# Performance work log

Measured on AMD Instinct MI355X. Metric: run time of the kernel, lower is better.

The kernel has to match this reference:

```python
import jax, jax.numpy as jnp
import numpy as np

BATCH, IN_DIM, LATENT, K = 16384, 768, 12288, 32

def setup_inputs() -> dict:
    key = jax.random.key(0)
    k1, k2, k3 = jax.random.split(key, 3)
    # kaiming-uniform-style scale for encoder/decoder weights
    enc_bound = float(np.sqrt(6.0 / IN_DIM))
    dec_bound = float(np.sqrt(6.0 / LATENT))
    x = jax.random.normal(k1, (BATCH, IN_DIM), dtype=jnp.float32)
    enc_w = jax.random.uniform(k2, (LATENT, IN_DIM), dtype=jnp.float32, minval=-enc_bound, maxval=enc_bound)
    enc_b = jnp.zeros((LATENT,), dtype=jnp.float32)
    dec_w = jax.random.uniform(k3, (IN_DIM, LATENT), dtype=jnp.float32, minval=-dec_bound, maxval=dec_bound)
    dec_b = jnp.zeros((IN_DIM,), dtype=jnp.float32)
    return {"x": x, "enc_w": enc_w, "enc_b": enc_b, "dec_w": dec_w, "dec_b": dec_b, "k": K}

def reference(x, enc_w, enc_b, dec_w, dec_b, k):
    # encode: z = x @ W_e^T + b_e            [B, LATENT]
    z = jnp.einsum('bi,li->bl', x, enc_w) + enc_b
    # top-k threshold: kth largest value per row, then shifted relu
    vals, _ = jax.lax.top_k(z, k)
    thresh = vals[:, -1:]                     # [B, 1]
    z_sparse = jax.nn.relu(z - thresh)
    # decode: dense GEMM over all latent columns (as in original module)
    x_recon = jnp.einsum('bl,il->bi', z_sparse, dec_w) + dec_b
    return (x_recon, z_sparse)
```

## Files before the change

### kernel.cpp

```cpp
#include <hip/hip_runtime.h>

#define M_DIM 16384
#define K_DIM 768
#define N_DIM 12288
#define TOPK  32
#define NCHUNK (N_DIM / 128)

typedef float f32x4 __attribute__((ext_vector_type(4)));
typedef short s16x8 __attribute__((ext_vector_type(8)));

__device__ __forceinline__ unsigned f2u(float f) {
  union { float f; unsigned u; } v; v.f = f; return v.u;
}
__device__ __forceinline__ float u2f(unsigned u) {
  union { unsigned u; float f; } v; v.u = u; return v.f;
}
__device__ __forceinline__ unsigned fkey(float f) {
  const unsigned u = f2u(f);
  return u ^ (unsigned)(((int)u >> 31) | 0x80000000);
}
__device__ __forceinline__ float kinv(unsigned k) {
  return u2f((k & 0x80000000u) ? (k ^ 0x80000000u) : ~k);
}
__device__ __forceinline__ unsigned short bf16_rne(float f) {
  unsigned u = f2u(f);
  return (unsigned short)((u + 0x7FFFu + ((u >> 16) & 1u)) >> 16);
}

__global__ __launch_bounds__(256) void TopKSparseAutoencoder_51917564674099_prep(
    const float* __restrict__ x, const float* __restrict__ w,
    const float* __restrict__ dw,
    unsigned short* __restrict__ xhi, unsigned short* __restrict__ xlo,
    unsigned short* __restrict__ whi, unsigned short* __restrict__ wlo,
    float* __restrict__ WT, int do_t, int do_s)
{
  __shared__ float tile[32][33];
  const int b = (int)blockIdx.x;
  const int t = (int)threadIdx.x;

  if (b < 9216) {
    if (!do_t) return;
    const int bx = b % (N_DIM / 32);
    const int by = b / (N_DIM / 32);
    const int tx = t & 31, ty = t >> 5;
#pragma unroll
    for (int j = 0; j < 32; j += 8)
      tile[ty + j][tx] = dw[(size_t)(by * 32 + ty + j) * N_DIM + bx * 32 + tx];
    __syncthreads();
#pragma unroll
    for (int j = 0; j < 32; j += 8)
      WT[(size_t)(bx * 32 + ty + j) * K_DIM + by * 32 + tx] = tile[tx][ty + j];
    return;
  }
  if (!do_s) return;

  const float* src; unsigned short* dh; unsigned short* dl; int i, stride, n4;
  if (b < 9216 + 1024) {
    src = x; dh = xhi; dl = xlo;
    i = (b - 9216) * 256 + t; stride = 1024 * 256; n4 = M_DIM * K_DIM / 4;
  } else {
    src = w; dh = whi; dl = wlo;
    i = (b - 10240) * 256 + t; stride = 512 * 256; n4 = N_DIM * K_DIM / 4;
  }
  for (; i < n4; i += stride) {
    const float4 v = ((const float4*)src)[i];
    ushort4 h, l;
    h.x = bf16_rne(v.x); h.y = bf16_rne(v.y); h.z = bf16_rne(v.z); h.w = bf16_rne(v.w);
    l.x = bf16_rne(v.x - u2f((unsigned)h.x << 16));
    l.y = bf16_rne(v.y - u2f((unsigned)h.y << 16));
    l.z = bf16_rne(v.z - u2f((unsigned)h.z << 16));
    l.w = bf16_rne(v.w - u2f((unsigned)h.w << 16));
    ((ushort4*)dh)[i] = h;
    ((ushort4*)dl)[i] = l;
  }
}

__device__ __forceinline__ void mfma16(f32x4& d, s16x8 a, s16x8 b) {
  asm("v_mfma_f32_16x16x32_bf16 %0, %1, %2, %0" : "+v"(d) : "v"(a), "v"(b));
}

#define GL16(g, l) __builtin_amdgcn_global_load_lds(                      \
    (const __attribute__((address_space(1))) void*)(g),                   \
    (__attribute__((address_space(3))) void*)(l), 16, 0, 0)

__global__ __launch_bounds__(256, 2) void TopKSparseAutoencoder_51917564674099_kernel(
    const unsigned short* __restrict__ Ahi, const unsigned short* __restrict__ Alo,
    const unsigned short* __restrict__ Bhi, const unsigned short* __restrict__ Blo,
    const float* __restrict__ bias, float* __restrict__ Z,
    float* __restrict__ cmax, int do_cmax)
{
  __shared__ unsigned short lds[4][128][32];
  __shared__ float cmx[128][2];

  const int t    = (int)threadIdx.x;
  const int wid  = t >> 6;
  const int lane = t & 63;

  const int bid  = (int)(blockIdx.y * gridDim.x + blockIdx.x);
  const int bswz = (bid & 7) * (12288 / 8) + (bid >> 3);
  const int n0   = (bswz % 96) * 128;
  const int m0   = (bswz / 96) * 128;

  const int rr  = lane >> 2;
  const int kq  = lane & 3;
  const int rt0 = wid * 32 + rr;
  const int rt1 = rt0 + 16;
  const int kc0 = (kq ^ ((rt0 >> 1) & 3)) * 8;
  const int kc1 = (kq ^ ((rt1 >> 1) & 3)) * 8;
  const size_t offA0 = (size_t)(m0 + rt0) * K_DIM + kc0;
  const size_t offA1 = (size_t)(m0 + rt1) * K_DIM + kc1;
  const size_t offB0 = (size_t)(n0 + rt0) * K_DIM + kc0;
  const size_t offB1 = (size_t)(n0 + rt1) * K_DIM + kc1;

  const int wm = (wid >> 1) * 64;
  const int wn = (wid & 1) * 64;
  const int lr = lane & 15;
  const int lc = lane >> 4;

  f32x4 acc[4][4];
#pragma unroll
  for (int i = 0; i < 4; ++i)
#pragma unroll
    for (int j = 0; j < 4; ++j) acc[i][j] = (f32x4){0.f, 0.f, 0.f, 0.f};

  for (int k0 = 0; k0 < K_DIM; k0 += 32) {
    GL16(Ahi + offA0 + k0, &lds[0][wid * 32][0]);
    GL16(Ahi + offA1 + k0, &lds[0][wid * 32 + 16][0]);
    GL16(Alo + offA0 + k0, &lds[1][wid * 32][0]);
    GL16(Alo + offA1 + k0, &lds[1][wid * 32 + 16][0]);
    GL16(Bhi + offB0 + k0, &lds[2][wid * 32][0]);
    GL16(Bhi + offB1 + k0, &lds[2][wid * 32 + 16][0]);
    GL16(Blo + offB0 + k0, &lds[3][wid * 32][0]);
    GL16(Blo + offB1 + k0, &lds[3][wid * 32 + 16][0]);
    __syncthreads();

    s16x8 ah[4], al[4], bh[4], bl[4];
#pragma unroll
    for (int i = 0; i < 4; ++i) {
      const int r = wm + i * 16 + lr;
      const int p = (lc ^ ((r >> 1) & 3)) * 8;
      ah[i] = *(const s16x8*)&lds[0][r][p];
      al[i] = *(const s16x8*)&lds[1][r][p];
    }
#pragma unroll
    for (int j = 0; j < 4; ++j) {
      const int r = wn + j * 16 + lr;
      const int p = (lc ^ ((r >> 1) & 3)) * 8;
      bh[j] = *(const s16x8*)&lds[2][r][p];
      bl[j] = *(const s16x8*)&lds[3][r][p];
    }
#pragma unroll
    for (int i = 0; i < 4; ++i)
#pragma unroll
      for (int j = 0; j < 4; ++j) {
        mfma16(acc[i][j], ah[i], bh[j]);
        mfma16(acc[i][j], ah[i], bl[j]);
        mfma16(acc[i][j], al[i], bh[j]);
      }
    __syncthreads();
  }

  asm volatile("s_nop 7\n\ts_nop 7" :::);

  float mx[4][4];
#pragma unroll
  for (int i = 0; i < 4; ++i)
#pragma unroll
    for (int q = 0; q < 4; ++q) mx[i][q] = -3.4e38f;

#pragma unroll
  for (int j = 0; j < 4; ++j) {
    const int col = n0 + wn + j * 16 + lr;
    const float bb = bias[col];
#pragma unroll
    for (int i = 0; i < 4; ++i) {
      const int r0 = m0 + wm + i * 16 + lc * 4;
#pragma unroll
      for (int q = 0; q < 4; ++q) {
        const float val = acc[i][j][q] + bb;
        Z[(size_t)(r0 + q) * N_DIM + col] = val;
        mx[i][q] = fmaxf(mx[i][q], val);
      }
    }
  }

  if (do_cmax) {
#pragma unroll
    for (int s = 1; s < 16; s <<= 1)
#pragma unroll
      for (int i = 0; i < 4; ++i)
#pragma unroll
        for (int q = 0; q < 4; ++q)
          mx[i][q] = fmaxf(mx[i][q], __shfl_xor(mx[i][q], s));
    if (lr == 0) {
#pragma unroll
      for (int i = 0; i < 4; ++i)
#pragma unroll
        for (int q = 0; q < 4; ++q)
          cmx[wm + i * 16 + lc * 4 + q][wid & 1] = mx[i][q];
    }
    __syncthreads();
    if (t < 128)
      cmax[(size_t)(m0 + t) * NCHUNK + (n0 >> 7)] = fmaxf(cmx[t][0], cmx[t][1]);
  }
}

__global__ void enc_gemm_f32_fb(
    const float* A, const float* B, const float* bias, float* Z)
{
  __shared__ float As[32][132];
  __shared__ float Bs[32][132];

  const int tx = (int)threadIdx.x;
  const int ty = (int)threadIdx.y;
  const int t  = ty * 16 + tx;
  const int n0 = (int)blockIdx.x * 128;
  const int m0 = (int)blockIdx.y * 128;
  const int r = t >> 1;
  const int h = (t & 1) * 16;

  float c[8][8];
#pragma unroll
  for (int i = 0; i < 8; ++i)
#pragma unroll
    for (int j = 0; j < 8; ++j) c[i][j] = 0.0f;

  for (int k0 = 0; k0 < K_DIM; k0 += 32) {
    const float* pa = A + (size_t)(m0 + r) * K_DIM + k0 + h;
    const float* pb = B + (size_t)(n0 + r) * K_DIM + k0 + h;
    float fa[16], fb[16];
#pragma unroll
    for (int j = 0; j < 16; ++j) fa[j] = pa[j];
#pragma unroll
    for (int j = 0; j < 16; ++j) fb[j] = pb[j];
#pragma unroll
    for (int j = 0; j < 16; ++j) As[h + j][r] = fa[j];
#pragma unroll
    for (int j = 0; j < 16; ++j) Bs[h + j][r] = fb[j];
    __syncthreads();

    for (int kk = 0; kk < 32; ++kk) {
      float av[8], bv[8];
#pragma unroll
      for (int i = 0; i < 8; ++i) av[i] = As[kk][ty * 8 + i];
#pragma unroll
      for (int j = 0; j < 8; ++j) bv[j] = Bs[kk][tx * 8 + j];
#pragma unroll
      for (int i = 0; i < 8; ++i)
#pragma unroll
        for (int j = 0; j < 8; ++j) c[i][j] += av[i] * bv[j];
    }
    __syncthreads();
  }

#pragma unroll
  for (int j = 0; j < 8; ++j) {
    const int col = n0 + tx * 8 + j;
    const float bb = bias[col];
#pragma unroll
    for (int i = 0; i < 8; ++i)
      Z[(size_t)(m0 + ty * 8 + i) * N_DIM + col] = c[i][j] + bb;
  }
}

__global__ __launch_bounds__(256, 4) void TopKSparseAutoencoder_51917564674099_zdecode(
    float* Z, const float* __restrict__ CMAX, const float* __restrict__ WT,
    const float* __restrict__ db, float* __restrict__ XR)
{
  __shared__ unsigned candk[4][256];
  __shared__ int      candi[4][256];
  __shared__ short    s_elig[4][NCHUNK];
  __shared__ int s_ne[4], s_cc[4], s_nnz[4];
  __shared__ int   s_col[4][TOPK];
  __shared__ float s_val[4][TOPK];

  const int t    = (int)threadIdx.x;
  const int lane = t & 63;
  const int wid  = t >> 6;
  const int row  = (int)blockIdx.x * 4 + wid;

  if (lane == 0) { s_ne[wid] = 0; s_cc[wid] = 0; s_nnz[wid] = 0; }
  if (lane < TOPK) { s_col[wid][lane] = 0; s_val[wid][lane] = 0.0f; }

  const f32x4* zr = (const f32x4*)(Z + (size_t)row * N_DIM);
  f32x4*       zw = (f32x4*)(Z + (size_t)row * N_DIM);

  const unsigned kA = fkey(CMAX[(size_t)row * NCHUNK + lane]);
  const unsigned kB = (lane < NCHUNK - 64) ? fkey(CMAX[(size_t)row * NCHUNK + 64 + lane]) : 0u;
  unsigned lo = 0;
  unsigned long long w = 1ULL << 32;
  for (int r = 0; r < 8; ++r) {
    w >>= 2;
    const unsigned wu = (unsigned)w;
    const unsigned m1 = lo + wu, m2 = lo + 2u * wu, m3 = lo + 3u * wu;
    unsigned p = (unsigned)((kA >= m1) + (kB >= m1)) |
                 ((unsigned)((kA >= m2) + (kB >= m2)) << 16);
    unsigned q = (unsigned)((kA >= m3) + (kB >= m3));
    p += __shfl_down(p, 32); q += __shfl_down(q, 32);
    p += __shfl_down(p, 16); q += __shfl_down(q, 16);
    p += __shfl_down(p, 8);  q += __shfl_down(q, 8);
    p += __shfl_down(p, 4);  q += __shfl_down(q, 4);
    p += __shfl_down(p, 2);  q += __shfl_down(q, 2);
    p += __shfl_down(p, 1);  q += __shfl_down(q, 1);
    p = __shfl(p, 0); q = __shfl(q, 0);
    if (q >= (unsigned)TOPK)                  lo = m3;
    else if ((p >> 16) >= (unsigned)TOPK)     lo = m2;
    else if ((p & 0xFFFFu) >= (unsigned)TOPK) lo = m1;
  }
  const unsigned B = lo;

  if (kA >= B) { const int p = atomicAdd(&s_ne[wid], 1); s_elig[wid][p] = (short)lane; }
  if (lane < NCHUNK - 64 && kB >= B) {
    const int p = atomicAdd(&s_ne[wid], 1); s_elig[wid][p] = (short)(lane + 64);
  }
  const int ne = s_ne[wid];

  for (int i = (lane >> 5); i < ne; i += 2) {
    const int c  = (int)s_elig[wid][i];
    const int f4 = (c << 5) + (lane & 31);
    const f32x4 v = zr[f4];
    const int base = f4 << 2;
    const unsigned k0 = fkey(v[0]), k1 = fkey(v[1]), k2 = fkey(v[2]), k3 = fkey(v[3]);
    if (k0 >= B) { int p = atomicAdd(&s_cc[wid], 1); if (p < 256) { candk[wid][p] = k0; candi[wid][p] = base; } }
    if (k1 >= B) { int p = atomicAdd(&s_cc[wid], 1); if (p < 256) { candk[wid][p] = k1; candi[wid][p] = base + 1; } }
    if (k2 >= B) { int p = atomicAdd(&s_cc[wid], 1); if (p < 256) { candk[wid][p] = k2; candi[wid][p] = base + 2; } }
    if (k3 >= B) { int p = atomicAdd(&s_cc[wid], 1); if (p < 256) { candk[wid][p] = k3; candi[wid][p] = base + 3; } }
  }
  const int cc = s_cc[wid];
  const f32x4 z4 = (f32x4){0.f, 0.f, 0.f, 0.f};

  if (cc <= 256) {
#pragma unroll 8
    for (int jj = 0; jj < 48; ++jj) zw[lane + 64 * jj] = z4;

    unsigned k[4];
#pragma unroll
    for (int i = 0; i < 4; ++i) k[i] = (lane + 64 * i < cc) ? candk[wid][lane + 64 * i] : 0u;
    lo = 0; w = 1ULL << 32;
    for (int r = 0; r < 16; ++r) {
      w >>= 2;
      const unsigned wu = (unsigned)w;
      const unsigned m1 = lo + wu, m2 = lo + 2u * wu, m3 = lo + 3u * wu;
      unsigned c1 = 0, c2 = 0, c3 = 0;
#pragma unroll
      for (int i = 0; i < 4; ++i) { c1 += (k[i] >= m1); c2 += (k[i] >= m2); c3 += (k[i] >= m3); }
      unsigned p = c1 | (c2 << 16), q = c3;
      p += __shfl_down(p, 32); q += __shfl_down(q, 32);
      p += __shfl_down(p, 16); q += __shfl_down(q, 16);
      p += __shfl_down(p, 8);  q += __shfl_down(q, 8);
      p += __shfl_down(p, 4);  q += __shfl_down(q, 4);
      p += __shfl_down(p, 2);  q += __shfl_down(q, 2);
      p += __shfl_down(p, 1);  q += __shfl_down(q, 1);
      p = __shfl(p, 0); q = __shfl(q, 0);
      if (q >= (unsigned)TOPK)                  lo = m3;
      else if ((p >> 16) >= (unsigned)TOPK)     lo = m2;
      else if ((p & 0xFFFFu) >= (unsigned)TOPK) lo = m1;
    }
    const unsigned T = lo;
    const float thresh = kinv(T);
    for (int i = lane; i < cc; i += 64) {
      const unsigned ck = candk[wid][i];
      if (ck > T) {
        const int p = atomicAdd(&s_nnz[wid], 1);
        if (p < TOPK) { s_col[wid][p] = candi[wid][i]; s_val[wid][p] = kinv(ck) - thresh; }
      }
    }
  } else {
    lo = 0; w = 1ULL << 32;
    for (int r = 0; r < 16; ++r) {
      w >>= 2;
      const unsigned wu = (unsigned)w;
      const unsigned m1 = lo + wu, m2 = lo + 2u * wu, m3 = lo + 3u * wu;
      unsigned c1 = 0, c2 = 0, c3 = 0;
      for (int j = 0; j < 48; ++j) {
        const f32x4 v = zr[lane + 64 * j];
        const unsigned k0 = fkey(v[0]), k1 = fkey(v[1]), k2 = fkey(v[2]), k3 = fkey(v[3]);
        c1 += (k0 >= m1) + (k1 >= m1) + (k2 >= m1) + (k3 >= m1);
        c2 += (k0 >= m2) + (k1 >= m2) + (k2 >= m2) + (k3 >= m2);
        c3 += (k0 >= m3) + (k1 >= m3) + (k2 >= m3) + (k3 >= m3);
      }
      unsigned p = c1 | (c2 << 16), q = c3;
      p += __shfl_down(p, 32); q += __shfl_down(q, 32);
      p += __shfl_down(p, 16); q += __shfl_down(q, 16);
      p += __shfl_down(p, 8);  q += __shfl_down(q, 8);
      p += __shfl_down(p, 4);  q += __shfl_down(q, 4);
      p += __shfl_down(p, 2);  q += __shfl_down(q, 2);
      p += __shfl_down(p, 1);  q += __shfl_down(q, 1);
      p = __shfl(p, 0); q = __shfl(q, 0);
      if (q >= (unsigned)TOPK)                  lo = m3;
      else if ((p >> 16) >= (unsigned)TOPK)     lo = m2;
      else if ((p & 0xFFFFu) >= (unsigned)TOPK) lo = m1;
    }
    const unsigned T = lo;
    const float thresh = kinv(T);
    for (int j = 0; j < 48; ++j) {
      const f32x4 v = zr[lane + 64 * j];
      const int base = (lane + 64 * j) * 4;
      const unsigned k0 = fkey(v[0]), k1 = fkey(v[1]), k2 = fkey(v[2]), k3 = fkey(v[3]);
      if (k0 > T) { int p = atomicAdd(&s_nnz[wid], 1); if (p < TOPK) { s_col[wid][p] = base;     s_val[wid][p] = kinv(k0) - thresh; } }
      if (k1 > T) { int p = atomicAdd(&s_nnz[wid], 1); if (p < TOPK) { s_col[wid][p] = base + 1; s_val[wid][p] = kinv(k1) - thresh; } }
      if (k2 > T) { int p = atomicAdd(&s_nnz[wid], 1); if (p < TOPK) { s_col[wid][p] = base + 2; s_val[wid][p] = kinv(k2) - thresh; } }
      if (k3 > T) { int p = atomicAdd(&s_nnz[wid], 1); if (p < TOPK) { s_col[wid][p] = base + 3; s_val[wid][p] = kinv(k3) - thresh; } }
      zw[lane + 64 * j] = z4;
    }
  }

  asm volatile("s_waitcnt vmcnt(0)" ::: "memory");
  const int nnz = (s_nnz[wid] < TOPK) ? s_nnz[wid] : TOPK;
  if (lane < nnz) Z[(size_t)row * N_DIM + s_col[wid][lane]] = s_val[wid][lane];

  const f32x4* WT4 = (const f32x4*)WT;
  f32x4 a0 = z4, a1 = z4, a2 = z4;
#pragma unroll 4
  for (int j = 0; j < TOPK; ++j) {
    const float v = s_val[wid][j];
    const size_t base = (size_t)s_col[wid][j] * (K_DIM / 4);
    const f32x4 w0 = WT4[base + lane];
    const f32x4 w1 = WT4[base + 64 + lane];
    const f32x4 w2 = WT4[base + 128 + lane];
    a0 += w0 * v;
    a1 += w1 * v;
    a2 += w2 * v;
  }
  const f32x4* db4 = (const f32x4*)db;
  f32x4* xr4 = (f32x4*)(XR + (size_t)row * K_DIM);
  xr4[lane]        = a0 + db4[lane];
  xr4[64 + lane]   = a1 + db4[64 + lane];
  xr4[128 + lane]  = a2 + db4[128 + lane];
}

__device__ __forceinline__ void full_round_l(
    const uint4* zk, unsigned red[][2][4], int t, int lane, int wid, int r,
    unsigned& lo, unsigned long long& w)
{
  w >>= 2;
  const unsigned wu = (unsigned)w;
  const unsigned m1 = lo + wu, m2 = lo + 2u * wu, m3 = lo + 3u * wu;
  unsigned c1 = 0, c2 = 0, c3 = 0;
#pragma unroll
  for (int j = 0; j < 12; ++j) {
    const uint4 k = zk[t + 256 * j];
    c1 += (k.x >= m1) + (k.y >= m1) + (k.z >= m1) + (k.w >= m1);
    c2 += (k.x >= m2) + (k.y >= m2) + (k.z >= m2) + (k.w >= m2);
    c3 += (k.x >= m3) + (k.y >= m3) + (k.z >= m3) + (k.w >= m3);
  }
  unsigned p = c1 | (c2 << 16), q = c3;
  p += __shfl_down(p, 32); q += __shfl_down(q, 32);
  p += __shfl_down(p, 16); q += __shfl_down(q, 16);
  p += __shfl_down(p, 8);  q += __shfl_down(q, 8);
  p += __shfl_down(p, 4);  q += __shfl_down(q, 4);
  p += __shfl_down(p, 2);  q += __shfl_down(q, 2);
  p += __shfl_down(p, 1);  q += __shfl_down(q, 1);
  const int par = r & 1;
  if (lane == 0) { red[par][0][wid] = p; red[par][1][wid] = q; }
  __syncthreads();
  const unsigned P = red[par][0][0] + red[par][0][1] + red[par][0][2] + red[par][0][3];
  const unsigned Q = red[par][1][0] + red[par][1][1] + red[par][1][2] + red[par][1][3];
  if (Q >= (unsigned)TOPK)                lo = m3;
  else if ((P >> 16) >= (unsigned)TOPK)   lo = m2;
  else if ((P & 0xFFFFu) >= (unsigned)TOPK) lo = m1;
}

__global__ __launch_bounds__(256, 3) void topk_select_decode_fb(
    float* Z, const float* __restrict__ WT, const float* __restrict__ DW,
    const float* __restrict__ db, float* __restrict__ XR, int use_wt)
{
  __shared__ uint4 zkey4[N_DIM / 4];
  __shared__ unsigned red[2][2][4];
  __shared__ unsigned cand[256];
  __shared__ unsigned s_T;
  __shared__ int s_cc;
  __shared__ int s_nnz;
  __shared__ int   s_col[TOPK];
  __shared__ float s_val[TOPK];

  const int row  = (int)blockIdx.x;
  const int t    = (int)threadIdx.x;
  const int lane = t & 63;
  const int wid  = t >> 6;

  float4* zv = (float4*)(Z + (size_t)row * N_DIM);

#pragma unroll
  for (int j = 0; j < 12; ++j) {
    const float4 v = zv[t + 256 * j];
    uint4 k;
    k.x = fkey(v.x); k.y = fkey(v.y); k.z = fkey(v.z); k.w = fkey(v.w);
    zkey4[t + 256 * j] = k;
  }
  if (t == 0) { s_nnz = 0; s_cc = 0; }
  if (t < TOPK) { s_col[t] = 0; s_val[t] = 0.0f; }
  __syncthreads();

  unsigned lo = 0;
  unsigned long long w = 1ULL << 32;
  for (int r = 0; r < 8; ++r)
    full_round_l(zkey4, red, t, lane, wid, r, lo, w);

#pragma unroll
  for (int j = 0; j < 12; ++j) {
    const uint4 k = zkey4[t + 256 * j];
    if (k.x >= lo) { int p = atomicAdd(&s_cc, 1); if (p < 256) cand[p] = k.x; }
    if (k.y >= lo) { int p = atomicAdd(&s_cc, 1); if (p < 256) cand[p] = k.y; }
    if (k.z >= lo) { int p = atomicAdd(&s_cc, 1); if (p < 256) cand[p] = k.z; }
    if (k.w >= lo) { int p = atomicAdd(&s_cc, 1); if (p < 256) cand[p] = k.w; }
  }
  __syncthreads();
  const int cc = s_cc;

  if (cc <= 256) {
    if (wid == 0) {
      const unsigned k0 = (lane       < cc) ? cand[lane]       : 0u;
      const unsigned k1 = (lane + 64  < cc) ? cand[lane + 64]  : 0u;
      const unsigned k2 = (lane + 128 < cc) ? cand[lane + 128] : 0u;
      const unsigned k3 = (lane + 192 < cc) ? cand[lane + 192] : 0u;
      for (int r = 8; r < 16; ++r) {
        w >>= 2;
        const unsigned wu = (unsigned)w;
        const unsigned m1 = lo + wu, m2 = lo + 2u * wu, m3 = lo + 3u * wu;
        unsigned c1 = (k0 >= m1) + (k1 >= m1) + (k2 >= m1) + (k3 >= m1);
        unsigned c2 = (k0 >= m2) + (k1 >= m2) + (k2 >= m2) + (k3 >= m2);
        unsigned c3 = (k0 >= m3) + (k1 >= m3) + (k2 >= m3) + (k3 >= m3);
        unsigned p = c1 | (c2 << 16), q = c3;
        p += __shfl_down(p, 32); q += __shfl_down(q, 32);
        p += __shfl_down(p, 16); q += __shfl_down(q, 16);
        p += __shfl_down(p, 8);  q += __shfl_down(q, 8);
        p += __shfl_down(p, 4);  q += __shfl_down(q, 4);
        p += __shfl_down(p, 2);  q += __shfl_down(q, 2);
        p += __shfl_down(p, 1);  q += __shfl_down(q, 1);
        p = __shfl(p, 0); q = __shfl(q, 0);
        if (q >= (unsigned)TOPK)                  lo = m3;
        else if ((p >> 16) >= (unsigned)TOPK)     lo = m2;
        else if ((p & 0xFFFFu) >= (unsigned)TOPK) lo = m1;
      }
      if (lane == 0) s_T = lo;
    }
  } else {
    for (int r = 8; r < 16; ++r)
      full_round_l(zkey4, red, t, lane, wid, r, lo, w);
    if (t == 0) s_T = lo;
  }
  __syncthreads();
  const unsigned T = s_T;
  const float thresh = kinv(T);

#define COMPF(KF, OFS, OF) {                                                  \
      float v = 0.0f;                                                         \
      if (KF > T) {                                                           \
        v = kinv(KF) - thresh;                                                \
        const int p = atomicAdd(&s_nnz, 1);                                   \
        if (p < TOPK) { s_col[p] = base + OFS; s_val[p] = v; }                \
      }                                                                       \
      o.OF = v; }
#pragma unroll
  for (int j = 0; j < 12; ++j) {
    const uint4 k = zkey4[t + 256 * j];
    const int base = (t + 256 * j) * 4;
    float4 o;
    COMPF(k.x, 0, x)
    COMPF(k.y, 1, y)
    COMPF(k.z, 2, z)
    COMPF(k.w, 3, w)
    zv[t + 256 * j] = o;
  }
#undef COMPF
  __syncthreads();

  float a0 = 0.0f, a1 = 0.0f, a2 = 0.0f;
  if (use_wt) {
#pragma unroll 8
    for (int j = 0; j < TOPK; ++j) {
      const float v = s_val[j];
      const float* wp = WT + (size_t)s_col[j] * K_DIM;
      a0 += v * wp[t];
      a1 += v * wp[t + 256];
      a2 += v * wp[t + 512];
    }
  } else {
#pragma unroll 8
    for (int j = 0; j < TOPK; ++j) {
      const float v = s_val[j];
      const int col = s_col[j];
      a0 += v * DW[(size_t)(t)       * N_DIM + col];
      a1 += v * DW[(size_t)(t + 256) * N_DIM + col];
      a2 += v * DW[(size_t)(t + 512) * N_DIM + col];
    }
  }
  float* xr = XR + (size_t)row * K_DIM;
  xr[t]       = a0 + db[t];
  xr[t + 256] = a1 + db[t + 256];
  xr[t + 512] = a2 + db[t + 512];
}

extern "C" void kernel_launch(void* const* d_in, const int* in_sizes, int n_in,
                              void* d_out, int out_size, void* d_ws, size_t ws_size,
                              hipStream_t stream)
{
  (void)in_sizes; (void)n_in; (void)out_size;

  const float* x     = (const float*)d_in[0];
  const float* enc_w = (const float*)d_in[1];
  const float* enc_b = (const float*)d_in[2];
  const float* dec_w = (const float*)d_in[3];
  const float* dec_b = (const float*)d_in[4];

  float* out     = (float*)d_out;
  float* x_recon = out;
  float* z_sp    = out + (size_t)M_DIM * K_DIM;

  const size_t WT_BYTES = (size_t)N_DIM * K_DIM * sizeof(float);
  const size_t XPLANE   = (size_t)M_DIM * K_DIM * sizeof(unsigned short);
  const size_t WPLANE   = (size_t)N_DIM * K_DIM * sizeof(unsigned short);
  const size_t FULL     = WT_BYTES + 2 * XPLANE + 2 * WPLANE;
  const size_t CMAX_B   = (size_t)M_DIM * NCHUNK * sizeof(float);
  const size_t FULL2    = FULL + CMAX_B;

  char* ws = (char*)d_ws;
  const int use_wt   = (ws_size >= WT_BYTES) ? 1 : 0;
  const int use_mfma = (ws_size >= FULL) ? 1 : 0;
  const int use_cmax = (ws_size >= FULL2) ? 1 : 0;

  float*          WT   = (float*)ws;
  unsigned short* xhi  = (unsigned short*)(ws + WT_BYTES);
  unsigned short* xlo  = (unsigned short*)(ws + WT_BYTES + XPLANE);
  unsigned short* whi  = (unsigned short*)(ws + WT_BYTES + 2 * XPLANE);
  unsigned short* wlo  = (unsigned short*)(ws + WT_BYTES + 2 * XPLANE + WPLANE);
  float*          CMAX = (float*)(ws + FULL);

  if (use_wt || use_mfma)
    TopKSparseAutoencoder_51917564674099_prep<<<10752, 256, 0, stream>>>(
        x, enc_w, dec_w, xhi, xlo, whi, wlo, WT, use_wt, use_mfma);

  if (use_mfma) {
    dim3 tg(N_DIM / 128, M_DIM / 128);
    TopKSparseAutoencoder_51917564674099_kernel<<<tg, 256, 0, stream>>>(
        xhi, xlo, whi, wlo, enc_b, z_sp, CMAX, use_cmax);
  } else {
    dim3 tb(16, 16);
    dim3 tg(N_DIM / 128, M_DIM / 128);
    enc_gemm_f32_fb<<<tg, tb, 0, stream>>>(x, enc_w, enc_b, z_sp);
  }

  if (use_cmax)
    TopKSparseAutoencoder_51917564674099_zdecode<<<M_DIM / 4, 256, 0, stream>>>(
        z_sp, CMAX, WT, dec_b, x_recon);
  else
    topk_select_decode_fb<<<M_DIM, 256, 0, stream>>>(
        z_sp, WT, dec_w, dec_b, x_recon, use_wt);
}
```

Baseline: 2.170 ms.

## Enlarge encoder GEMM tile to 256x256 with double-buffered LDS pipeline

Moves the split-bf16 MFMA encoder GEMM from 128x128 tiles with 256 threads to 256x256 tiles with 512 threads (8 waves, each computing 128x64). It adds two LDS buffers with explicit vmcnt waits, so global-to-LDS loads of the next k-slice overlap the MFMAs on the current one, and raises wave priority around the MFMA block. The goal is more data reuse per loaded byte and hidden load latency, at the cost of more registers (32 accumulators), more LDS and one block per CU. The column-max epilogue is adjusted to write two 128-wide chunks per block.

```diff
diff --git a/kernel.cpp b/kernel.cpp
--- a/kernel.cpp
+++ b/kernel.cpp
@@ -83,23 +83,24 @@
     (const __attribute__((address_space(1))) void*)(g),                   \
     (__attribute__((address_space(3))) void*)(l), 16, 0, 0)
 
-__global__ __launch_bounds__(256, 2) void TopKSparseAutoencoder_51917564674099_kernel(
+__global__ __launch_bounds__(512, 1) void TopKSparseAutoencoder_51917564674099_kernel(
     const unsigned short* __restrict__ Ahi, const unsigned short* __restrict__ Alo,
     const unsigned short* __restrict__ Bhi, const unsigned short* __restrict__ Blo,
     const float* __restrict__ bias, float* __restrict__ Z,
     float* __restrict__ cmax, int do_cmax)
 {
-  __shared__ unsigned short lds[4][128][32];
-  __shared__ float cmx[128][2];
+  __shared__ unsigned short lA[2][2][256][32];
+  __shared__ unsigned short lB[2][2][256][32];
+  __shared__ float cmx[256][2][2];
 
   const int t    = (int)threadIdx.x;
   const int wid  = t >> 6;
   const int lane = t & 63;
 
   const int bid  = (int)(blockIdx.y * gridDim.x + blockIdx.x);
-  const int bswz = (bid & 7) * (12288 / 8) + (bid >> 3);
-  const int n0   = (bswz % 96) * 128;
-  const int m0   = (bswz / 96) * 128;
+  const int bswz = (bid & 7) * (3072 / 8) + (bid >> 3);
+  const int n0   = (bswz % 48) * 256;
+  const int m0   = (bswz / 48) * 256;
 
   const int rr  = lane >> 2;
   const int kq  = lane & 3;
@@ -112,59 +113,85 @@
   const size_t offB0 = (size_t)(n0 + rt0) * K_DIM + kc0;
   const size_t offB1 = (size_t)(n0 + rt1) * K_DIM + kc1;
 
-  const int wm = (wid >> 1) * 64;
-  const int wn = (wid & 1) * 64;
+  const int wm = (wid >> 2) * 128;
+  const int wn = (wid & 3) * 64;
   const int lr = lane & 15;
   const int lc = lane >> 4;
 
-  f32x4 acc[4][4];
-#pragma unroll
-  for (int i = 0; i < 4; ++i)
+  f32x4 acc[8][4];
+#pragma unroll
+  for (int i = 0; i < 8; ++i)
 #pragma unroll
     for (int j = 0; j < 4; ++j) acc[i][j] = (f32x4){0.f, 0.f, 0.f, 0.f};
 
-  for (int k0 = 0; k0 < K_DIM; k0 += 32) {
-    GL16(Ahi + offA0 + k0, &lds[0][wid * 32][0]);
-    GL16(Ahi + offA1 + k0, &lds[0][wid * 32 + 16][0]);
-    GL16(Alo + offA0 + k0, &lds[1][wid * 32][0]);
-    GL16(Alo + offA1 + k0, &lds[1][wid * 32 + 16][0]);
-    GL16(Bhi + offB0 + k0, &lds[2][wid * 32][0]);
-    GL16(Bhi + offB1 + k0, &lds[2][wid * 32 + 16][0]);
-    GL16(Blo + offB0 + k0, &lds[3][wid * 32][0]);
-    GL16(Blo + offB1 + k0, &lds[3][wid * 32 + 16][0]);
-    __syncthreads();
-
-    s16x8 ah[4], al[4], bh[4], bl[4];
-#pragma unroll
-    for (int i = 0; i < 4; ++i) {
-      const int r = wm + i * 16 + lr;
-      const int p = (lc ^ ((r >> 1) & 3)) * 8;
-      ah[i] = *(const s16x8*)&lds[0][r][p];
-      al[i] = *(const s16x8*)&lds[1][r][p];
-    }
-#pragma unroll
-    for (int j = 0; j < 4; ++j) {
-      const int r = wn + j * 16 + lr;
-      const int p = (lc ^ ((r >> 1) & 3)) * 8;
-      bh[j] = *(const s16x8*)&lds[2][r][p];
-      bl[j] = *(const s16x8*)&lds[3][r][p];
-    }
-#pragma unroll
-    for (int i = 0; i < 4; ++i)
-#pragma unroll
-      for (int j = 0; j < 4; ++j) {
-        mfma16(acc[i][j], ah[i], bh[j]);
-        mfma16(acc[i][j], ah[i], bl[j]);
-        mfma16(acc[i][j], al[i], bh[j]);
-      }
-    __syncthreads();
-  }
+#define STG(B, KO) do {                                              \
+    GL16(Ahi + offA0 + (KO), &lA[B][0][wid * 32][0]);                \
+    GL16(Ahi + offA1 + (KO), &lA[B][0][wid * 32 + 16][0]);           \
+    GL16(Alo + offA0 + (KO), &lA[B][1][wid * 32][0]);                \
+    GL16(Alo + offA1 + (KO), &lA[B][1][wid * 32 + 16][0]);           \
+    GL16(Bhi + offB0 + (KO), &lB[B][0][wid * 32][0]);                \
+    GL16(Bhi + offB1 + (KO), &lB[B][0][wid * 32 + 16][0]);           \
+    GL16(Blo + offB0 + (KO), &lB[B][1][wid * 32][0]);                \
+    GL16(Blo + offB1 + (KO), &lB[B][1][wid * 32 + 16][0]);           \
+  } while (0)
+
+#define COMPUTE(B) do {                                              \
+    s16x8 ah[8], al[8], bh[4], bl[4];                                \
+    _Pragma("unroll")                                                \
+    for (int i = 0; i < 8; ++i) {                                    \
+      const int r = wm + i * 16 + lr;                                \
+      const int p = (lc ^ ((r >> 1) & 3)) * 8;                       \
+      ah[i] = *(const s16x8*)&lA[B][0][r][p];                        \
+      al[i] = *(const s16x8*)&lA[B][1][r][p];                        \
+    }                                                                \
+    _Pragma("unroll")                                                \
+    for (int j = 0; j < 4; ++j) {                                    \
+      const int r = wn + j * 16 + lr;                                \
+      const int p = (lc ^ ((r >> 1) & 3)) * 8;                       \
+      bh[j] = *(const s16x8*)&lB[B][0][r][p];                        \
+      bl[j] = *(const s16x8*)&lB[B][1][r][p];                        \
+    }                                                                \
+    __builtin_amdgcn_s_setprio(1);                                   \
+    _Pragma("unroll")                                                \
+    for (int i = 0; i < 8; ++i)                                      \
+    _Pragma("unroll")                                                \
+      for (int j = 0; j < 4; ++j) {                                  \
+        mfma16(acc[i][j], ah[i], bh[j]);                             \
+        mfma16(acc[i][j], ah[i], bl[j]);                             \
+        mfma16(acc[i][j], al[i], bh[j]);                             \
+      }                                                              \
+    __builtin_amdgcn_s_setprio(0);                                   \
+  } while (0)
+
+  STG(0, 0);
+  STG(1, 32);
+  asm volatile("s_waitcnt vmcnt(8)" ::: "memory");
+  __builtin_amdgcn_s_barrier();
+  __builtin_amdgcn_sched_barrier(0);
+
+  for (int tt = 0; tt < 22; ++tt) {
+    const int cb = tt & 1;
+    COMPUTE(cb);
+    __builtin_amdgcn_s_barrier();
+    __builtin_amdgcn_sched_barrier(0);
+    STG(cb, (tt + 2) * 32);
+    asm volatile("s_waitcnt vmcnt(8)" ::: "memory");
+    __builtin_amdgcn_s_barrier();
+    __builtin_amdgcn_sched_barrier(0);
+  }
+  COMPUTE(0);
+  asm volatile("s_waitcnt vmcnt(0)" ::: "memory");
+  __builtin_amdgcn_s_barrier();
+  __builtin_amdgcn_sched_barrier(0);
+  COMPUTE(1);
+#undef STG
+#undef COMPUTE
 
   asm volatile("s_nop 7\n\ts_nop 7" :::);
 
-  float mx[4][4];
-#pragma unroll
-  for (int i = 0; i < 4; ++i)
+  float mx[8][4];
+#pragma unroll
+  for (int i = 0; i < 8; ++i)
 #pragma unroll
     for (int q = 0; q < 4; ++q) mx[i][q] = -3.4e38f;
 
@@ -173,7 +200,7 @@
     const int col = n0 + wn + j * 16 + lr;
     const float bb = bias[col];
 #pragma unroll
-    for (int i = 0; i < 4; ++i) {
+    for (int i = 0; i < 8; ++i) {
       const int r0 = m0 + wm + i * 16 + lc * 4;
 #pragma unroll
       for (int q = 0; q < 4; ++q) {
@@ -188,20 +215,25 @@
 #pragma unroll
     for (int s = 1; s < 16; s <<= 1)
 #pragma unroll
-      for (int i = 0; i < 4; ++i)
+      for (int i = 0; i < 8; ++i)
 #pragma unroll
         for (int q = 0; q < 4; ++q)
           mx[i][q] = fmaxf(mx[i][q], __shfl_xor(mx[i][q], s));
     if (lr == 0) {
-#pragma unroll
-      for (int i = 0; i < 4; ++i)
+      const int c = wn >> 7;
+      const int h = (wn >> 6) & 1;
+#pragma unroll
+      for (int i = 0; i < 8; ++i)
 #pragma unroll
         for (int q = 0; q < 4; ++q)
-          cmx[wm + i * 16 + lc * 4 + q][wid & 1] = mx[i][q];
+          cmx[wm + i * 16 + lc * 4 + q][c][h] = mx[i][q];
     }
     __syncthreads();
-    if (t < 128)
-      cmax[(size_t)(m0 + t) * NCHUNK + (n0 >> 7)] = fmaxf(cmx[t][0], cmx[t][1]);
+    if (t < 256) {
+      const size_t rb = (size_t)(m0 + t) * NCHUNK + (n0 >> 7);
+      cmax[rb]     = fmaxf(cmx[t][0][0], cmx[t][0][1]);
+      cmax[rb + 1] = fmaxf(cmx[t][1][0], cmx[t][1][1]);
+    }
   }
 }
 
@@ -632,8 +664,8 @@
         x, enc_w, dec_w, xhi, xlo, whi, wlo, WT, use_wt, use_mfma);
 
   if (use_mfma) {
-    dim3 tg(N_DIM / 128, M_DIM / 128);
-    TopKSparseAutoencoder_51917564674099_kernel<<<tg, 256, 0, stream>>>(
+    dim3 tg(N_DIM / 256, M_DIM / 256);
+    TopKSparseAutoencoder_51917564674099_kernel<<<tg, 512, 0, stream>>>(
         xhi, xlo, whi, wlo, enc_b, z_sp, CMAX, use_cmax);
   } else {
     dim3 tb(16, 16);
```

Measured after the change: 2.076 ms. -4.3%, faster.
